# Optimization experiments

Hardware: AMD Instinct MI355X
Metric: run time of the kernel (lower is better)

## Reference

```python
import jax, jax.numpy as jnp
import numpy as np

N, E = 50000, 800000          # nodes, edges (avg degree 16)
D_IN, D_H, D_OUT = 128, 128, 64
BN_EPS = 1e-5


def setup_inputs() -> dict:
    key = jax.random.key(0)
    ks = jax.random.split(key, 8)
    g = lambda k, shp, s: jax.random.normal(k, shp, jnp.float32) * s
    return {
        "x": jax.random.normal(ks[0], (N, D_IN), jnp.float32),
        "edge_index": jax.random.randint(ks[1], (2, E), 0, N),
        # SAGEConv layer 1: lin_l (neighbors, with bias), lin_r (root, no bias)
        "Wl1": g(ks[2], (D_IN, D_H), 0.05),
        "Wr1": g(ks[3], (D_IN, D_H), 0.05),
        "b1": jnp.zeros((D_H,), jnp.float32),
        # BatchNorm1d(hidden)
        "gamma": jnp.ones((D_H,), jnp.float32),
        "beta": jnp.zeros((D_H,), jnp.float32),
        # SAGEConv layer 2
        "Wl2": g(ks[4], (D_H, D_OUT), 0.05),
        "Wr2": g(ks[5], (D_H, D_OUT), 0.05),
        "b2": jnp.zeros((D_OUT,), jnp.float32),
    }


def _sage_conv(x, src, dst, Wl, Wr, b):
    """PyG SAGEConv (mean aggr): lin_l(mean_{j in N(i)} x_j) + lin_r(x_i)."""
    n = x.shape[0]
    agg = jax.ops.segment_sum(x[src], dst, num_segments=n)            # [N, d]
    cnt = jax.ops.segment_sum(jnp.ones((src.shape[0],), x.dtype), dst,
                              num_segments=n)                          # [N]
    agg = agg / jnp.maximum(cnt, 1.0)[:, None]                         # mean, 0 for isolated
    return agg @ Wl + x @ Wr + b


def _batch_norm(x, gamma, beta):
    """Training-mode BatchNorm1d: batch stats over the node axis, biased var."""
    mu = jnp.mean(x, axis=0)
    var = jnp.var(x, axis=0)
    return gamma * (x - mu) * jax.lax.rsqrt(var + BN_EPS) + beta


def reference(x, edge_index, Wl1, Wr1, b1, gamma, beta, Wl2, Wr2, b2):
    src, dst = edge_index[0], edge_index[1]
    h = _sage_conv(x, src, dst, Wl1, Wr1, b1)
    h = jax.nn.relu(_batch_norm(h, gamma, beta))
    # dropout is identity in eval / deterministic reference
    return _sage_conv(h, src, dst, Wl2, Wr2, b2)
```

## Files before the change

kernel.cpp:

```cpp
#include <hip/hip_runtime.h>
#include <hip/hip_bf16.h>
#include <hip/hip_fp8.h>

#define DIN   128
#define DH    128
#define DOUTC 64
#define BN_EPS 1e-5f

typedef __attribute__((ext_vector_type(8))) short bf16x8;
typedef __attribute__((ext_vector_type(4))) float f32x4;
typedef __attribute__((ext_vector_type(2))) float f32x2;

#ifndef __has_builtin
#define __has_builtin(x) 0
#endif
#if __has_builtin(__builtin_amdgcn_cvt_pk_f32_fp8) && __has_builtin(__builtin_amdgcn_cvt_pk_fp8_f32)
#define HW_FP8 1
#else
#define HW_FP8 0
#endif

__device__ inline unsigned short f2bf(float f) {
    __hip_bfloat16 b = __float2bfloat16(f);
    return *reinterpret_cast<unsigned short*>(&b);
}
__device__ inline float bf2f(unsigned short u) {
    return __uint_as_float(((unsigned int)u) << 16);
}
__device__ inline void fp8x4_to_f32(unsigned int w, float* o) {
#if HW_FP8
    f32x2 lo = __builtin_amdgcn_cvt_pk_f32_fp8((int)w, false);
    f32x2 hi = __builtin_amdgcn_cvt_pk_f32_fp8((int)w, true);
    o[0] = lo.x; o[1] = lo.y; o[2] = hi.x; o[3] = hi.y;
#else
    #pragma unroll
    for (int c = 0; c < 4; ++c) {
        __hip_fp8_e4m3 q; q.__x = (__hip_fp8_storage_t)((w >> (8 * c)) & 0xFF);
        o[c] = (float)q;
    }
#endif
}
__device__ inline unsigned int f32x4_to_fp8(float a, float b, float c, float d) {
#if HW_FP8
    int p = __builtin_amdgcn_cvt_pk_fp8_f32(a, b, 0, false);
    p = __builtin_amdgcn_cvt_pk_fp8_f32(c, d, p, true);
    return (unsigned int)p;
#else
    __hip_fp8_e4m3 qa(a), qb(b), qc(c), qd(d);
    return (unsigned int)qa.__x | ((unsigned int)qb.__x << 8) |
           ((unsigned int)qc.__x << 16) | ((unsigned int)qd.__x << 24);
#endif
}

__device__ inline void block_excl_scan_256(const int* __restrict__ arr,
                                           int* __restrict__ excl,
                                           int* __restrict__ wsum, int tid)
{
    int lane = tid & 63, w = tid >> 6;
    int v = arr[tid];
    int inc = v;
    #pragma unroll
    for (int off = 1; off < 64; off <<= 1) {
        int t = __shfl_up(inc, off, 64);
        if (lane >= off) inc += t;
    }
    if (lane == 63) wsum[w] = inc;
    __syncthreads();
    if (tid == 0) {
        int s = 0;
        #pragma unroll
        for (int i = 0; i < 4; ++i) { int t = wsum[i]; wsum[i] = s; s += t; }
    }
    __syncthreads();
    excl[tid] = inc - v + wsum[w];
    __syncthreads();
}

__device__ inline void block_excl_scan_256_w1024(const int* __restrict__ arr,
                                                 int* __restrict__ excl,
                                                 int* __restrict__ wsum, int tid)
{
    int lane = tid & 63, w = tid >> 6;
    int v = (tid < 256) ? arr[tid] : 0;
    int inc = v;
    #pragma unroll
    for (int off = 1; off < 64; off <<= 1) {
        int t = __shfl_up(inc, off, 64);
        if (lane >= off) inc += t;
    }
    if (w < 4 && lane == 63) wsum[w] = inc;
    __syncthreads();
    if (tid == 0) {
        int s = 0;
        #pragma unroll
        for (int i = 0; i < 4; ++i) { int t = wsum[i]; wsum[i] = s; s += t; }
    }
    __syncthreads();
    if (tid < 256) excl[tid] = inc - v + wsum[w];
    __syncthreads();
}

__global__ __launch_bounds__(256) void prep_kernel(
    const float* __restrict__ x, unsigned char* __restrict__ xq,
    unsigned short* __restrict__ xb,
    const float* __restrict__ Wl1, const float* __restrict__ Wr1,
    const float* __restrict__ Wl2, const float* __restrict__ Wr2,
    unsigned short* __restrict__ W1p, unsigned short* __restrict__ W2p,
    const int* __restrict__ ei, int* __restrict__ cursor,
    unsigned int* __restrict__ coarse,
    int total8, int cvtB, int E, int nb, int cap)
{
    __shared__ int hist[256], lstart[256], gbase[256], wsum[4];
    __shared__ unsigned int staged[4096];
    const int b = blockIdx.x;
    const int tid = threadIdx.x;

    if (b < cvtB) {
        int i = b * 256 + tid;
        if (i >= total8) return;
        float4 a = ((const float4*)x)[2 * i];
        float4 c = ((const float4*)x)[2 * i + 1];
        uint2 pk;
        pk.x = f32x4_to_fp8(a.x, a.y, a.z, a.w);
        pk.y = f32x4_to_fp8(c.x, c.y, c.z, c.w);
        *(uint2*)(xq + (size_t)i * 8) = pk;
        unsigned short t8[8];
        t8[0]=f2bf(a.x); t8[1]=f2bf(a.y); t8[2]=f2bf(a.z); t8[3]=f2bf(a.w);
        t8[4]=f2bf(c.x); t8[5]=f2bf(c.y); t8[6]=f2bf(c.z); t8[7]=f2bf(c.w);
        *(uint4*)(xb + (size_t)i * 8) = *(uint4*)t8;
        return;
    }
    if (b < cvtB + 192) {
        int region = (b - cvtB) >> 6;
        int idx = ((b - cvtB) & 63) * 256 + tid;
        int k = idx >> 7, c = idx & 127;
        int d = ((k >> 5) * 8 + (c >> 4)) * 512 + ((k >> 3) & 3) * 128 + (c & 15) * 8 + (k & 7);
        if (region == 0)      W1p[d] = f2bf(Wl1[idx]);
        else if (region == 1) W1p[128 * 128 + d] = f2bf(Wr1[idx]);
        else {
            float v = (c < 64) ? Wl2[k * 64 + c] : Wr2[k * 64 + (c - 64)];
            W2p[d] = f2bf(v);
        }
        return;
    }

    const int chunkBase = (b - cvtB - 192) * 4096;
    hist[tid] = 0;
    __syncthreads();

    unsigned int rec[16]; int pos[16]; int bb[16];
    #pragma unroll
    for (int i = 0; i < 16; ++i) {
        int e = chunkBase + i * 256 + tid;
        if (e < E) {
            int s = ei[e], d = ei[E + e];
            rec[i] = ((unsigned int)d << 16) | (unsigned int)s;
            bb[i]  = d >> 8;
            pos[i] = atomicAdd(&hist[bb[i]], 1);
        } else bb[i] = -1;
    }
    __syncthreads();

    block_excl_scan_256(hist, lstart, wsum, tid);

    if (tid < nb) {
        int c = hist[tid];
        gbase[tid] = c ? atomicAdd(&cursor[tid], c) : 0;
    }
    __syncthreads();

    #pragma unroll
    for (int i = 0; i < 16; ++i)
        if (bb[i] >= 0) staged[lstart[bb[i]] + pos[i]] = rec[i];
    __syncthreads();

    int total = min(4096, E - chunkBase);
    for (int i = tid; i < total; i += 256) {
        unsigned int r = staged[i];
        int bk  = (int)(r >> 24);
        int gp  = gbase[bk] + (i - lstart[bk]);
        if (gp < cap) coarse[(size_t)bk * cap + gp] = r;
    }
}

__global__ __launch_bounds__(1024) void bin_fine(
    const int* __restrict__ cursor, const unsigned int* __restrict__ coarse,
    unsigned short* __restrict__ sorted, int* __restrict__ deg,
    int* __restrict__ row_start, int n, int cap)
{
    __shared__ int hist[256], pstart[256], cur2[256], wsum[4];
    const int b = blockIdx.x, tid = threadIdx.x;
    const int cnt = min(cursor[b], cap);
    const unsigned int* src = coarse + (size_t)b * cap;

    if (tid < 256) hist[tid] = 0;
    __syncthreads();

    int nIter = (cnt + 1023) >> 10;
    for (int i = 0; i < nIter; ++i) {
        int idx = i * 1024 + tid;
        if (idx < cnt) atomicAdd(&hist[(src[idx] >> 16) & 255], 1);
    }
    __syncthreads();

    block_excl_scan_256_w1024(hist, pstart, wsum, tid);
    if (tid < 256) cur2[tid] = pstart[tid];
    __syncthreads();

    for (int i = 0; i < nIter; ++i) {
        int idx = i * 1024 + tid;
        if (idx < cnt) {
            unsigned int r = src[idx];
            int dl = (r >> 16) & 255;
            int p  = atomicAdd(&cur2[dl], 1);
            sorted[(size_t)b * cap + p] = (unsigned short)(r & 0xFFFFu);
        }
    }

    int node = b * 256 + tid;
    if (tid < 256 && node < n) {
        deg[node]       = hist[tid];
        row_start[node] = b * cap + pstart[tid];
    }
}

__global__ __launch_bounds__(256) void gemm1_fused(
    const unsigned char* __restrict__ xq, const unsigned short* __restrict__ xb,
    const int* __restrict__ row_start, const int* __restrict__ deg,
    const unsigned short* __restrict__ sorted,
    const unsigned short* __restrict__ W1p, const float* __restrict__ bias,
    unsigned short* __restrict__ hb,
    float* __restrict__ bn_part, int n)
{
    __shared__ unsigned short G[32][136];
    __shared__ float red[2][2][128];

    const int block_row = blockIdx.x * 32;
    const int tid  = threadIdx.x;
    const int wave = tid >> 6;
    const int lane = tid & 63;
    const int q    = lane >> 4;
    const int m16  = lane & 15;
    const int rg   = wave >> 1;
    const int ch   = wave & 1;

    {
        int sub = lane & 7, oct = lane >> 3;
        int lr = rg * 16 + ch * 8 + oct;
        int g  = block_row + lr;
        float acc[16];
        #pragma unroll
        for (int j = 0; j < 16; ++j) acc[j] = 0.f;
        int d = 0, base = 0;
        if (g < n) { base = row_start[g]; d = deg[g]; }
        int nb8 = (d + 7) >> 3;
        int si[8];
        if (nb8 > 0) {
            #pragma unroll
            for (int u = 0; u < 8; ++u)
                si[u] = (int)sorted[base + (u < d ? u : 0)];
        }
        for (int b = 0; b < nb8; ++b) {
            uint4 raws[8];
            #pragma unroll
            for (int u = 0; u < 8; ++u)
                raws[u] = ((const uint4*)(xq + (size_t)si[u] * DIN))[sub];
            if (b + 1 < nb8) {
                int t0n = (b + 1) * 8;
                #pragma unroll
                for (int u = 0; u < 8; ++u) {
                    int tt = t0n + u;
                    si[u] = (int)sorted[base + (tt < d ? tt : 0)];
                }
            }
            int t0 = b * 8;
            #pragma unroll
            for (int u = 0; u < 8; ++u) {
                float w8 = (t0 + u < d) ? 1.0f : 0.0f;
                const unsigned int* w = (const unsigned int*)&raws[u];
                #pragma unroll
                for (int c = 0; c < 4; ++c) {
                    float o4[4];
                    fp8x4_to_f32(w[c], o4);
                    acc[c*4+0] = fmaf(o4[0], w8, acc[c*4+0]);
                    acc[c*4+1] = fmaf(o4[1], w8, acc[c*4+1]);
                    acc[c*4+2] = fmaf(o4[2], w8, acc[c*4+2]);
                    acc[c*4+3] = fmaf(o4[3], w8, acc[c*4+3]);
                }
            }
        }
        float inv = 1.0f / fmaxf((float)d, 1.0f);
        unsigned short t16[16];
        #pragma unroll
        for (int j = 0; j < 16; ++j) t16[j] = f2bf(acc[j] * inv);
        *(uint4*)&G[lr][sub * 16]     = ((uint4*)t16)[0];
        *(uint4*)&G[lr][sub * 16 + 8] = ((uint4*)t16)[1];
    }
    __syncthreads();

    f32x4 acc[4];
    #pragma unroll
    for (int nt = 0; nt < 4; ++nt) acc[nt] = (f32x4){0.f, 0.f, 0.f, 0.f};

    const int grow = block_row + rg * 16 + m16;
    #pragma unroll
    for (int ks = 0; ks < 4; ++ks) {
        bf16x8 ag = *(const bf16x8*)&G[rg * 16 + m16][ks * 32 + q * 8];
        const unsigned short* wp0 = W1p + (size_t)ks * 8 * 512 + (size_t)ch * 4 * 512;
        #pragma unroll
        for (int nt = 0; nt < 4; ++nt) {
            bf16x8 b = *(const bf16x8*)(wp0 + nt * 512 + lane * 8);
            acc[nt] = __builtin_amdgcn_mfma_f32_16x16x32_bf16(ag, b, acc[nt], 0, 0, 0);
        }
        uint4 raw = make_uint4(0u, 0u, 0u, 0u);
        if (grow < n)
            raw = *(const uint4*)(xb + (size_t)grow * DIN + ks * 32 + q * 8);
        bf16x8 ax = *(bf16x8*)&raw;
        const unsigned short* wp1 = W1p + (size_t)(4 + ks) * 8 * 512 + (size_t)ch * 4 * 512;
        #pragma unroll
        for (int nt = 0; nt < 4; ++nt) {
            bf16x8 b = *(const bf16x8*)(wp1 + nt * 512 + lane * 8);
            acc[nt] = __builtin_amdgcn_mfma_f32_16x16x32_bf16(ax, b, acc[nt], 0, 0, 0);
        }
    }

    float psum[4], psq[4];
    #pragma unroll
    for (int nt = 0; nt < 4; ++nt) {
        int col = (ch * 4 + nt) * 16 + m16;
        float bv = bias[col];
        float s = 0.f, ssq = 0.f;
        #pragma unroll
        for (int reg = 0; reg < 4; ++reg) {
            int g = block_row + rg * 16 + q * 4 + reg;
            float v = acc[nt][reg] + bv;
            if (g < n) {
                hb[(size_t)g * DH + col] = f2bf(v);
                s += v; ssq += v * v;
            }
        }
        psum[nt] = s; psq[nt] = ssq;
    }
    #pragma unroll
    for (int nt = 0; nt < 4; ++nt) {
        psum[nt] += __shfl_xor(psum[nt], 16, 64);
        psum[nt] += __shfl_xor(psum[nt], 32, 64);
        psq[nt]  += __shfl_xor(psq[nt], 16, 64);
        psq[nt]  += __shfl_xor(psq[nt], 32, 64);
    }
    if (lane < 16) {
        #pragma unroll
        for (int nt = 0; nt < 4; ++nt) {
            red[0][rg][(ch * 4 + nt) * 16 + lane] = psum[nt];
            red[1][rg][(ch * 4 + nt) * 16 + lane] = psq[nt];
        }
    }
    __syncthreads();
    if (tid < 128) {
        float s   = red[0][0][tid] + red[0][1][tid];
        float ssq = red[1][0][tid] + red[1][1][tid];
        bn_part[(size_t)blockIdx.x * 256 + tid]       = s;
        bn_part[(size_t)blockIdx.x * 256 + 128 + tid] = ssq;
    }
}

__global__ __launch_bounds__(256) void bn_reduce(
    const float* __restrict__ bn_part, float* __restrict__ bn_out, int nblk)
{
    const int tid = threadIdx.x;
    float s = 0.f;
    for (int r = blockIdx.x; r < nblk; r += 64)
        s += bn_part[(size_t)r * 256 + tid];
    atomicAdd(&bn_out[tid], s);
}

__global__ __launch_bounds__(256) void gemm2p_mfma(
    const unsigned short* __restrict__ hb,
    const float* __restrict__ bn_sum, const float* __restrict__ bn_sumsq,
    const float* __restrict__ gamma, const float* __restrict__ beta,
    const unsigned short* __restrict__ W2p, const float* __restrict__ bias,
    unsigned short* __restrict__ P, float* __restrict__ out, int n)
{
    __shared__ float s_scale[128], s_shift[128];

    const int block_row = blockIdx.x * 64;
    const int tid  = threadIdx.x;
    const int wave = tid >> 6;
    const int lane = tid & 63;
    const int q    = lane >> 4;
    const int m16  = lane & 15;

    if (tid < 128) {
        float invN = 1.0f / (float)n;
        float mu  = bn_sum[tid] * invN;
        float var = bn_sumsq[tid] * invN - mu * mu;
        float sc  = gamma[tid] * rsqrtf(var + BN_EPS);
        s_scale[tid] = sc;
        s_shift[tid] = beta[tid] - mu * sc;
    }
    __syncthreads();

    f32x4 acc[8];
    #pragma unroll
    for (int nt = 0; nt < 8; ++nt) acc[nt] = (f32x4){0.f, 0.f, 0.f, 0.f};

    const int grow = block_row + wave * 16 + m16;
    #pragma unroll
    for (int ks = 0; ks < 4; ++ks) {
        bf16x8 a;
        {
            int kbase = ks * 32 + q * 8;
            float4 sc0 = *(const float4*)&s_scale[kbase];
            float4 sc1 = *(const float4*)&s_scale[kbase + 4];
            float4 sh0 = *(const float4*)&s_shift[kbase];
            float4 sh1 = *(const float4*)&s_shift[kbase + 4];
            unsigned short t[8] = {0,0,0,0,0,0,0,0};
            if (grow < n) {
                uint4 raw = *(const uint4*)(hb + (size_t)grow * DH + kbase);
                const unsigned short* u = (const unsigned short*)&raw;
                t[0] = f2bf(fmaxf(bf2f(u[0]) * sc0.x + sh0.x, 0.f));
                t[1] = f2bf(fmaxf(bf2f(u[1]) * sc0.y + sh0.y, 0.f));
                t[2] = f2bf(fmaxf(bf2f(u[2]) * sc0.z + sh0.z, 0.f));
                t[3] = f2bf(fmaxf(bf2f(u[3]) * sc0.w + sh0.w, 0.f));
                t[4] = f2bf(fmaxf(bf2f(u[4]) * sc1.x + sh1.x, 0.f));
                t[5] = f2bf(fmaxf(bf2f(u[5]) * sc1.y + sh1.y, 0.f));
                t[6] = f2bf(fmaxf(bf2f(u[6]) * sc1.z + sh1.z, 0.f));
                t[7] = f2bf(fmaxf(bf2f(u[7]) * sc1.w + sh1.w, 0.f));
            }
            a = *(bf16x8*)t;
        }
        const unsigned short* wp = W2p + (size_t)ks * 8 * 512;
        #pragma unroll
        for (int nt = 0; nt < 8; ++nt) {
            bf16x8 b = *(const bf16x8*)(wp + nt * 512 + lane * 8);
            acc[nt] = __builtin_amdgcn_mfma_f32_16x16x32_bf16(a, b, acc[nt], 0, 0, 0);
        }
    }

    #pragma unroll
    for (int nt = 0; nt < 4; ++nt) {
        int col = nt * 16 + m16;
        #pragma unroll
        for (int reg = 0; reg < 4; ++reg) {
            int g = block_row + wave * 16 + q * 4 + reg;
            if (g < n) P[(size_t)g * DOUTC + col] = f2bf(acc[nt][reg]);
        }
    }
    #pragma unroll
    for (int nt = 4; nt < 8; ++nt) {
        int col = (nt - 4) * 16 + m16;
        float bv = bias[col];
        #pragma unroll
        for (int reg = 0; reg < 4; ++reg) {
            int g = block_row + wave * 16 + q * 4 + reg;
            if (g < n) out[(size_t)g * DOUTC + col] = acc[nt][reg] + bv;
        }
    }
}

__global__ __launch_bounds__(256) void agg_gather64_add(
    const int* __restrict__ row_start, const int* __restrict__ deg,
    const unsigned short* __restrict__ sorted, const unsigned short* __restrict__ P,
    float* __restrict__ out, int n)
{
    int wid  = (blockIdx.x * 256 + threadIdx.x) >> 6;
    int lane = threadIdx.x & 63;
    int sub = lane & 7, oct = lane >> 3;
    int r = wid * 8 + oct;
    if (r >= n) return;

    float acc[8];
    #pragma unroll
    for (int j = 0; j < 8; ++j) acc[j] = 0.f;

    int base = row_start[r];
    int d    = deg[r];
    int nb8  = (d + 7) >> 3;
    int si[8];
    if (nb8 > 0) {
        #pragma unroll
        for (int u = 0; u < 8; ++u)
            si[u] = (int)sorted[base + (u < d ? u : 0)];
    }
    for (int b = 0; b < nb8; ++b) {
        uint4 raws[8];
        #pragma unroll
        for (int u = 0; u < 8; ++u)
            raws[u] = ((const uint4*)(P + (size_t)si[u] * DOUTC))[sub];
        if (b + 1 < nb8) {
            int t0n = (b + 1) * 8;
            #pragma unroll
            for (int u = 0; u < 8; ++u) {
                int tt = t0n + u;
                si[u] = (int)sorted[base + (tt < d ? tt : 0)];
            }
        }
        int t0 = b * 8;
        #pragma unroll
        for (int u = 0; u < 8; ++u) {
            float w8 = (t0 + u < d) ? 1.0f : 0.0f;
            const unsigned short* us = (const unsigned short*)&raws[u];
            #pragma unroll
            for (int j = 0; j < 8; ++j) acc[j] = fmaf(bf2f(us[j]), w8, acc[j]);
        }
    }
    float inv = 1.0f / fmaxf((float)d, 1.0f);
    float* op = out + (size_t)r * DOUTC + sub * 8;
    float4 c0 = *(float4*)op;
    float4 c1 = *((float4*)op + 1);
    c0.x += acc[0] * inv; c0.y += acc[1] * inv;
    c0.z += acc[2] * inv; c0.w += acc[3] * inv;
    c1.x += acc[4] * inv; c1.y += acc[5] * inv;
    c1.z += acc[6] * inv; c1.w += acc[7] * inv;
    *(float4*)op = c0;
    *((float4*)op + 1) = c1;
}

extern "C" void kernel_launch(void* const* d_in, const int* in_sizes, int n_in,
                              void* d_out, int out_size, void* d_ws, size_t ws_size,
                              hipStream_t stream)
{
    const float* x     = (const float*)d_in[0];
    const int*   ei    = (const int*)  d_in[1];
    const float* Wl1   = (const float*)d_in[2];
    const float* Wr1   = (const float*)d_in[3];
    const float* b1    = (const float*)d_in[4];
    const float* gamma = (const float*)d_in[5];
    const float* beta  = (const float*)d_in[6];
    const float* Wl2   = (const float*)d_in[7];
    const float* Wr2   = (const float*)d_in[8];
    const float* b2    = (const float*)d_in[9];
    float*       out   = (float*)d_out;

    const int N = in_sizes[0] / DIN;
    const int E = in_sizes[1] / 2;

    const int NB  = (N + 255) >> 8;
    int cap = (E / NB) * 3 / 2 + 256;
    cap = (cap + 255) & ~255;

    const int gemm1_blocks = (N + 31) / 32;
    const int gemm2_blocks = (N + 63) / 64;

    float* bn_sum   = (float*)d_ws;
    float* bn_sumsq = bn_sum + DH;
    int* cursor     = (int*)(bn_sumsq + DH);
    int* deg        = cursor + 256;
    int* row_start  = deg + N;
    unsigned int* coarse   = (unsigned int*)(row_start + N);
    unsigned short* sorted = (unsigned short*)(coarse + (size_t)NB * cap);
    unsigned short* hb     = sorted + (size_t)NB * cap;
    unsigned short* P      = hb + (size_t)N * DH;
    unsigned short* W1p    = P + (size_t)N * DOUTC;
    unsigned short* W2p    = W1p + 256 * 128;
    unsigned short* xb     = W2p + 128 * 128;
    unsigned char*  xq     = (unsigned char*)(xb + (size_t)N * DIN);
    float* bn_part  = (float*)(xq + (size_t)N * DIN);

    hipMemsetAsync(bn_sum, 0, (2 * DH + 256) * sizeof(float), stream);

    dim3 blk(256);
    const int cvtB        = (N * DIN / 8 + 255) / 256;
    const int binA_blocks = (E + 4095) / 4096;
    const int g64_blocks  = ((N + 7) / 8 + 3) / 4;

    prep_kernel<<<cvtB + 192 + binA_blocks, blk, 0, stream>>>(
        x, xq, xb, Wl1, Wr1, Wl2, Wr2, W1p, W2p,
        ei, cursor, coarse, N * DIN / 8, cvtB, E, NB, cap);

    bin_fine<<<NB, dim3(1024), 0, stream>>>(cursor, coarse, sorted, deg,
                                            row_start, N, cap);

    gemm1_fused<<<gemm1_blocks, blk, 0, stream>>>(xq, xb, row_start, deg, sorted,
                                                  W1p, b1, hb, bn_part, N);

    bn_reduce<<<64, blk, 0, stream>>>(bn_part, bn_sum, gemm1_blocks);

    gemm2p_mfma<<<gemm2_blocks, blk, 0, stream>>>(hb, bn_sum, bn_sumsq,
                                                  gamma, beta, W2p, b2, P, out, N);

    agg_gather64_add<<<g64_blocks, blk, 0, stream>>>(row_start, deg, sorted,
                                                     P, out, N);
}
```

Measured before the change: 185.6 us.

## Reorder prep blocks to bin edges first and split gemm2 columns across waves

The prep kernel's block order changes so the edge-binning blocks come first. These are the long-latency blocks with atomics and scans, so they now dispatch early instead of trailing after the conversion blocks. gemm2 now covers 32 rows per block instead of 64, and two waves split the 128 output columns (P half and out half). This doubles the block count and halves the accumulators per wave, which should raise parallelism and occupancy. The cost is that each A row's BN/ReLU/bf16 conversion is now done by two waves instead of one.

```diff
diff --git a/kernel.cpp b/kernel.cpp
--- a/kernel.cpp
+++ b/kernel.cpp
@@ -108,31 +108,32 @@
     unsigned short* __restrict__ W1p, unsigned short* __restrict__ W2p,
     const int* __restrict__ ei, int* __restrict__ cursor,
     unsigned int* __restrict__ coarse,
-    int total8, int cvtB, int E, int nb, int cap)
+    int total8, int binA, int cvtB, int E, int nb, int cap)
 {
     __shared__ int hist[256], lstart[256], gbase[256], wsum[4];
     __shared__ unsigned int staged[4096];
     const int b = blockIdx.x;
     const int tid = threadIdx.x;
 
-    if (b < cvtB) {
-        int i = b * 256 + tid;
-        if (i >= total8) return;
-        float4 a = ((const float4*)x)[2 * i];
-        float4 c = ((const float4*)x)[2 * i + 1];
-        uint2 pk;
-        pk.x = f32x4_to_fp8(a.x, a.y, a.z, a.w);
-        pk.y = f32x4_to_fp8(c.x, c.y, c.z, c.w);
-        *(uint2*)(xq + (size_t)i * 8) = pk;
-        unsigned short t8[8];
-        t8[0]=f2bf(a.x); t8[1]=f2bf(a.y); t8[2]=f2bf(a.z); t8[3]=f2bf(a.w);
-        t8[4]=f2bf(c.x); t8[5]=f2bf(c.y); t8[6]=f2bf(c.z); t8[7]=f2bf(c.w);
-        *(uint4*)(xb + (size_t)i * 8) = *(uint4*)t8;
-        return;
-    }
-    if (b < cvtB + 192) {
-        int region = (b - cvtB) >> 6;
-        int idx = ((b - cvtB) & 63) * 256 + tid;
+    if (b >= binA) {
+        int b2 = b - binA;
+        if (b2 < cvtB) {
+            int i = b2 * 256 + tid;
+            if (i >= total8) return;
+            float4 a = ((const float4*)x)[2 * i];
+            float4 c = ((const float4*)x)[2 * i + 1];
+            uint2 pk;
+            pk.x = f32x4_to_fp8(a.x, a.y, a.z, a.w);
+            pk.y = f32x4_to_fp8(c.x, c.y, c.z, c.w);
+            *(uint2*)(xq + (size_t)i * 8) = pk;
+            unsigned short t8[8];
+            t8[0]=f2bf(a.x); t8[1]=f2bf(a.y); t8[2]=f2bf(a.z); t8[3]=f2bf(a.w);
+            t8[4]=f2bf(c.x); t8[5]=f2bf(c.y); t8[6]=f2bf(c.z); t8[7]=f2bf(c.w);
+            *(uint4*)(xb + (size_t)i * 8) = *(uint4*)t8;
+            return;
+        }
+        int region = (b2 - cvtB) >> 6;
+        int idx = ((b2 - cvtB) & 63) * 256 + tid;
         int k = idx >> 7, c = idx & 127;
         int d = ((k >> 5) * 8 + (c >> 4)) * 512 + ((k >> 3) & 3) * 128 + (c & 15) * 8 + (k & 7);
         if (region == 0)      W1p[d] = f2bf(Wl1[idx]);
@@ -144,7 +145,7 @@
         return;
     }
 
-    const int chunkBase = (b - cvtB - 192) * 4096;
+    const int chunkBase = b * 4096;
     hist[tid] = 0;
     __syncthreads();
 
@@ -383,12 +384,14 @@
 {
     __shared__ float s_scale[128], s_shift[128];
 
-    const int block_row = blockIdx.x * 64;
+    const int block_row = blockIdx.x * 32;
     const int tid  = threadIdx.x;
     const int wave = tid >> 6;
     const int lane = tid & 63;
     const int q    = lane >> 4;
     const int m16  = lane & 15;
+    const int rg   = wave >> 1;
+    const int ch   = wave & 1;
 
     if (tid < 128) {
         float invN = 1.0f / (float)n;
@@ -400,11 +403,11 @@
     }
     __syncthreads();
 
-    f32x4 acc[8];
-    #pragma unroll
-    for (int nt = 0; nt < 8; ++nt) acc[nt] = (f32x4){0.f, 0.f, 0.f, 0.f};
-
-    const int grow = block_row + wave * 16 + m16;
+    f32x4 acc[4];
+    #pragma unroll
+    for (int nt = 0; nt < 4; ++nt) acc[nt] = (f32x4){0.f, 0.f, 0.f, 0.f};
+
+    const int grow = block_row + rg * 16 + m16;
     #pragma unroll
     for (int ks = 0; ks < 4; ++ks) {
         bf16x8 a;
@@ -429,31 +432,34 @@
             }
             a = *(bf16x8*)t;
         }
-        const unsigned short* wp = W2p + (size_t)ks * 8 * 512;
-        #pragma unroll
-        for (int nt = 0; nt < 8; ++nt) {
+        const unsigned short* wp = W2p + (size_t)ks * 8 * 512 + (size_t)ch * 4 * 512;
+        #pragma unroll
+        for (int nt = 0; nt < 4; ++nt) {
             bf16x8 b = *(const bf16x8*)(wp + nt * 512 + lane * 8);
             acc[nt] = __builtin_amdgcn_mfma_f32_16x16x32_bf16(a, b, acc[nt], 0, 0, 0);
         }
     }
 
-    #pragma unroll
-    for (int nt = 0; nt < 4; ++nt) {
-        int col = nt * 16 + m16;
-        #pragma unroll
-        for (int reg = 0; reg < 4; ++reg) {
-            int g = block_row + wave * 16 + q * 4 + reg;
-            if (g < n) P[(size_t)g * DOUTC + col] = f2bf(acc[nt][reg]);
-        }
-    }
-    #pragma unroll
-    for (int nt = 4; nt < 8; ++nt) {
-        int col = (nt - 4) * 16 + m16;
-        float bv = bias[col];
-        #pragma unroll
-        for (int reg = 0; reg < 4; ++reg) {
-            int g = block_row + wave * 16 + q * 4 + reg;
-            if (g < n) out[(size_t)g * DOUTC + col] = acc[nt][reg] + bv;
+    if (ch == 0) {
+        #pragma unroll
+        for (int nt = 0; nt < 4; ++nt) {
+            int col = nt * 16 + m16;
+            #pragma unroll
+            for (int reg = 0; reg < 4; ++reg) {
+                int g = block_row + rg * 16 + q * 4 + reg;
+                if (g < n) P[(size_t)g * DOUTC + col] = f2bf(acc[nt][reg]);
+            }
+        }
+    } else {
+        #pragma unroll
+        for (int nt = 0; nt < 4; ++nt) {
+            int col = nt * 16 + m16;
+            float bv = bias[col];
+            #pragma unroll
+            for (int reg = 0; reg < 4; ++reg) {
+                int g = block_row + rg * 16 + q * 4 + reg;
+                if (g < n) out[(size_t)g * DOUTC + col] = acc[nt][reg] + bv;
+            }
         }
     }
 }
@@ -540,7 +546,7 @@
     cap = (cap + 255) & ~255;
 
     const int gemm1_blocks = (N + 31) / 32;
-    const int gemm2_blocks = (N + 63) / 64;
+    const int gemm2_blocks = (N + 31) / 32;
 
     float* bn_sum   = (float*)d_ws;
     float* bn_sumsq = bn_sum + DH;
@@ -564,9 +570,9 @@
     const int binA_blocks = (E + 4095) / 4096;
     const int g64_blocks  = ((N + 7) / 8 + 3) / 4;
 
-    prep_kernel<<<cvtB + 192 + binA_blocks, blk, 0, stream>>>(
+    prep_kernel<<<binA_blocks + cvtB + 192, blk, 0, stream>>>(
         x, xq, xb, Wl1, Wr1, Wl2, Wr2, W1p, W2p,
-        ei, cursor, coarse, N * DIN / 8, cvtB, E, NB, cap);
+        ei, cursor, coarse, N * DIN / 8, binA_blocks, cvtB, E, NB, cap);
 
     bin_fine<<<NB, dim3(1024), 0, stream>>>(cursor, coarse, sorted, deg,
                                             row_start, N, cap);
```

Result: no change. 184.4 us (-0.6%).
